# Performance work log

Measured on AMD Instinct MI355X. Metric: run time of the kernel, lower is better.

The kernel has to match this reference:

```python
import jax, jax.numpy as jnp
import numpy as np

BETA = 0.5
N = 4096

def setup_inputs() -> dict:
    key = jax.random.key(0)
    k1, k2, k3 = jax.random.split(key, 3)
    A = jax.random.uniform(k1, (N, N), dtype=jnp.float32)
    h = jax.random.normal(k2, (N, N), dtype=jnp.float32)
    W = jax.random.normal(k3, (N, N), dtype=jnp.float32) * (1.0 / np.sqrt(N))
    return {"A": A, "h": h, "W": W}

def reference(A, h, W):
    # degrees from original A (before self-loops); D = diag(deg) + I is diagonal,
    # so torch.inverse(D) == elementwise reciprocal 1/(deg+1)
    deg = jnp.sum(A, axis=1)                       # [N]
    inv_d = 1.0 / (deg + 1.0)                      # [N]
    A_I = A + jnp.eye(A.shape[0], dtype=A.dtype)   # A += I
    # A_st = (A+I) @ diag(inv_d): scale columns
    A_st = A_I * inv_d[None, :]                    # [N,N]
    # A_st_11 = A_st @ h is dead code in the original (never used) -> skipped
    temp = BETA * h + (1.0 - BETA) * A_st          # [N,N]
    return temp @ W                                # [N,N]
```

## Files before the change

### kernel.cpp

```cpp
#include <hip/hip_runtime.h>
#include <hip/hip_bf16.h>

typedef unsigned short u16;
typedef unsigned int u32;
typedef __attribute__((ext_vector_type(8))) short bf16x8;
typedef __attribute__((ext_vector_type(4))) short s16x4;
typedef __attribute__((ext_vector_type(4))) float f32x4;

#define NN 4096

__device__ __forceinline__ u16 f2bf(float f) {
    union { float f; u32 u; } v; v.f = f;
    u32 r = v.u + 0x7fffu + ((v.u >> 16) & 1u);
    return (u16)(r >> 16);
}

__global__ void rowsum_kernel(const float* __restrict__ A, float* __restrict__ invd) {
    const int row = blockIdx.x;
    const float4* a4 = reinterpret_cast<const float4*>(A + (size_t)row * NN);
    float s = 0.f;
    #pragma unroll
    for (int i = 0; i < 4; ++i) {
        float4 v = a4[threadIdx.x + i * 256];
        s += v.x + v.y + v.z + v.w;
    }
    #pragma unroll
    for (int off = 32; off > 0; off >>= 1) s += __shfl_down(s, off, 64);
    __shared__ float ws[4];
    if ((threadIdx.x & 63) == 0) ws[threadIdx.x >> 6] = s;
    __syncthreads();
    if (threadIdx.x == 0) {
        float t = ws[0] + ws[1] + ws[2] + ws[3];
        invd[row] = 1.0f / (t + 1.0f);
    }
}

__global__ void make_temp_kernel(const float* __restrict__ A, const float* __restrict__ h,
                                 const float* __restrict__ invd, u16* __restrict__ T) {
    const size_t g = ((size_t)blockIdx.x * 256 + threadIdx.x) * 8;
    const int row = (int)(g >> 12);
    const int col = (int)(g & 4095);
    const float4* a4 = reinterpret_cast<const float4*>(A + g);
    const float4* h4 = reinterpret_cast<const float4*>(h + g);
    const float4* d4 = reinterpret_cast<const float4*>(invd + col);
    float4 a0 = a4[0], a1 = a4[1];
    float4 h0 = h4[0], h1 = h4[1];
    float4 dd0 = d4[0], dd1 = d4[1];
    float av[8] = {a0.x,a0.y,a0.z,a0.w,a1.x,a1.y,a1.z,a1.w};
    float hv[8] = {h0.x,h0.y,h0.z,h0.w,h1.x,h1.y,h1.z,h1.w};
    float dv[8] = {dd0.x,dd0.y,dd0.z,dd0.w,dd1.x,dd1.y,dd1.z,dd1.w};
    bf16x8 o;
    #pragma unroll
    for (int j = 0; j < 8; ++j) {
        float aa = av[j] + ((col + j == row) ? 1.0f : 0.0f);
        float t = 0.5f * hv[j] + 0.5f * aa * dv[j];
        o[j] = (short)f2bf(t);
    }
    *reinterpret_cast<bf16x8*>(T + g) = o;
}

__global__ void transposeW_kernel(const float* __restrict__ W, u16* __restrict__ Wt) {
    __shared__ float tile[64][65];
    const int nt = blockIdx.x & 63;
    const int kt = blockIdx.x >> 6;
    const int k0 = kt * 64, n0 = nt * 64;
    const int tr = threadIdx.x >> 4;
    const int tc = (threadIdx.x & 15) * 4;
    #pragma unroll
    for (int rr = 0; rr < 64; rr += 16) {
        float4 v = *reinterpret_cast<const float4*>(&W[(size_t)(k0 + tr + rr) * NN + n0 + tc]);
        tile[tr + rr][tc + 0] = v.x;
        tile[tr + rr][tc + 1] = v.y;
        tile[tr + rr][tc + 2] = v.z;
        tile[tr + rr][tc + 3] = v.w;
    }
    __syncthreads();
    #pragma unroll
    for (int rr = 0; rr < 64; rr += 16) {
        const int n = tr + rr;
        s16x4 o;
        #pragma unroll
        for (int j = 0; j < 4; ++j) o[j] = (short)f2bf(tile[tc + j][n]);
        *reinterpret_cast<s16x4*>(&Wt[(size_t)(n0 + n) * NN + k0 + tc]) = o;
    }
}


#define GLD16(g, l) __builtin_amdgcn_global_load_lds( \
    (const __attribute__((address_space(1))) void*)(g), \
    (__attribute__((address_space(3))) void*)(l), 16, 0, 0)

__global__ __launch_bounds__(512, 2) void gemm_kernel(
    const u16* __restrict__ Atl,
    const u16* __restrict__ Btl,
    float* __restrict__ C)
{
    __shared__ u16 S[4][2][8192];

    const int tid  = threadIdx.x;
    const int wid  = tid >> 6;
    const int lane = tid & 63;
    const int llo  = lane & 15;
    const int lhi  = lane >> 4;
    const int wr   = wid >> 2;
    const int wc   = wid & 3;

    const int swz = ((int)blockIdx.x & 7) * 32 + ((int)blockIdx.x >> 3);
    const int bm = swz >> 4, bn = swz & 15;
    const int tileRow = bm * 256, tileCol = bn * 256;

    const int r0 = tid >> 2;
    const int kc = (((tid & 3) ^ ((r0 >> 1) & 3)) << 3);
    const u16* gA0 = Atl + (size_t)(tileRow + r0) * NN + kc;
    const u16* gA1 = gA0 + (size_t)128 * NN;
    const u16* gB0 = Btl + (size_t)(tileCol + r0) * NN + kc;
    const u16* gB1 = gB0 + (size_t)128 * NN;

    int offA[8], offB[4];
    #pragma unroll
    for (int m = 0; m < 8; ++m) {
        const int row = wr * 128 + m * 16 + llo;
        offA[m] = row * 32 + ((lhi ^ ((row >> 1) & 3)) << 3);
    }
    #pragma unroll
    for (int n = 0; n < 4; ++n) {
        const int row = wc * 64 + n * 16 + llo;
        offB[n] = row * 32 + ((lhi ^ ((row >> 1) & 3)) << 3);
    }

    f32x4 acc[8][4];
    #pragma unroll
    for (int m = 0; m < 8; ++m)
        #pragma unroll
        for (int n = 0; n < 4; ++n)
            acc[m][n] = (f32x4){0.f, 0.f, 0.f, 0.f};

    #pragma unroll
    for (int p = 0; p < 3; ++p) {
        GLD16(gA0 + p * 32, &S[p][0][wid * 512]);
        GLD16(gA1 + p * 32, &S[p][0][4096 + wid * 512]);
        GLD16(gB0 + p * 32, &S[p][1][wid * 512]);
        GLD16(gB1 + p * 32, &S[p][1][4096 + wid * 512]);
    }
    gA0 += 96; gA1 += 96; gB0 += 96; gB1 += 96;
    asm volatile("s_waitcnt vmcnt(8)" ::: "memory");
    __builtin_amdgcn_s_barrier();
    asm volatile("" ::: "memory");

    #pragma unroll 1
    for (int t = 0; t < 128; ++t) {
        if (t < 125) {
            const int b3 = (t + 3) & 3;
            GLD16(gA0, &S[b3][0][wid * 512]);
            GLD16(gA1, &S[b3][0][4096 + wid * 512]);
            GLD16(gB0, &S[b3][1][wid * 512]);
            GLD16(gB1, &S[b3][1][4096 + wid * 512]);
            gA0 += 32; gA1 += 32; gB0 += 32; gB1 += 32;
        }
        __builtin_amdgcn_sched_barrier(0);

        const int b = t & 3;
        const u16* sA = &S[b][0][0];
        const u16* sB = &S[b][1][0];
        bf16x8 af[8], bv[4];
        #pragma unroll
        for (int m = 0; m < 8; ++m)
            af[m] = *reinterpret_cast<const bf16x8*>(sA + offA[m]);
        #pragma unroll
        for (int n = 0; n < 4; ++n)
            bv[n] = *reinterpret_cast<const bf16x8*>(sB + offB[n]);

        __builtin_amdgcn_s_setprio(1);
        #pragma unroll
        for (int m = 0; m < 8; ++m)
            #pragma unroll
            for (int n = 0; n < 4; ++n)
                acc[m][n] = __builtin_amdgcn_mfma_f32_16x16x32_bf16(
                    af[m], bv[n], acc[m][n], 0, 0, 0);
        __builtin_amdgcn_s_setprio(0);

        if (t < 125)       asm volatile("s_waitcnt vmcnt(8)" ::: "memory");
        else if (t == 125) asm volatile("s_waitcnt vmcnt(4)" ::: "memory");
        else if (t == 126) asm volatile("s_waitcnt vmcnt(0)" ::: "memory");
        if (t < 127) {
            __builtin_amdgcn_s_barrier();
            asm volatile("" ::: "memory");
        }
    }

    #pragma unroll
    for (int m = 0; m < 8; ++m) {
        #pragma unroll
        for (int n = 0; n < 4; ++n) {
            const size_t rbase = (size_t)(tileRow + wr * 128 + m * 16 + lhi * 4) * NN
                               + tileCol + wc * 64 + n * 16 + llo;
            #pragma unroll
            for (int j = 0; j < 4; ++j)
                C[rbase + (size_t)j * NN] = acc[m][n][j];
        }
    }
}

extern "C" void kernel_launch(void* const* d_in, const int* in_sizes, int n_in,
                              void* d_out, int out_size, void* d_ws, size_t ws_size,
                              hipStream_t stream) {
    const float* A = (const float*)d_in[0];
    const float* h = (const float*)d_in[1];
    const float* W = (const float*)d_in[2];
    float* out = (float*)d_out;

    float* invd = (float*)d_ws;
    u16* temp = (u16*)((char*)d_ws + 16384);
    u16* wt   = temp + (size_t)NN * NN;

    rowsum_kernel<<<NN, 256, 0, stream>>>(A, invd);
    make_temp_kernel<<<(NN * (size_t)NN) / (256 * 8), 256, 0, stream>>>(A, h, invd, temp);
    transposeW_kernel<<<(NN / 64) * (NN / 64), 256, 0, stream>>>(W, wt);
    gemm_kernel<<<256, 512, 0, stream>>>(temp, wt, out);
}
```

Measured before the change: 176.8 us.

## Restructure GEMM main loop into four-phase ping-pong with BK=64 staging

```diff
diff --git a/kernel.cpp b/kernel.cpp
--- a/kernel.cpp
+++ b/kernel.cpp
@@ -90,12 +90,23 @@
     (const __attribute__((address_space(1))) void*)(g), \
     (__attribute__((address_space(3))) void*)(l), 16, 0, 0)
 
+#define PHASE_MID  do { __builtin_amdgcn_sched_barrier(0); \
+    __builtin_amdgcn_s_barrier(); asm volatile("" ::: "memory"); } while (0)
+#define PHASE_END  do { __builtin_amdgcn_s_barrier(); \
+    asm volatile("" ::: "memory"); } while (0)
+
+__device__ __forceinline__ bf16x8 rd(const u16* base, int off, int ks) {
+    const u16* p = base + off;
+    if (ks) p = (const u16*)((uintptr_t)p ^ 64u);
+    return *reinterpret_cast<const bf16x8*>(p);
+}
+
 __global__ __launch_bounds__(512, 2) void gemm_kernel(
     const u16* __restrict__ Atl,
     const u16* __restrict__ Btl,
     float* __restrict__ C)
 {
-    __shared__ u16 S[4][2][8192];
+    __shared__ u16 S[2][4][8192];
 
     const int tid  = threadIdx.x;
     const int wid  = tid >> 6;
@@ -109,23 +120,28 @@
     const int bm = swz >> 4, bn = swz & 15;
     const int tileRow = bm * 256, tileCol = bn * 256;
 
-    const int r0 = tid >> 2;
-    const int kc = (((tid & 3) ^ ((r0 >> 1) & 3)) << 3);
-    const u16* gA0 = Atl + (size_t)(tileRow + r0) * NN + kc;
-    const u16* gA1 = gA0 + (size_t)128 * NN;
-    const u16* gB0 = Btl + (size_t)(tileCol + r0) * NN + kc;
-    const u16* gB1 = gB0 + (size_t)128 * NN;
+    const int srow = tid >> 3;
+    const int skg  = (((tid & 7) ^ ((tid >> 4) & 7)) << 3);
+    const size_t R64  = (size_t)64 * NN;
+    const size_t R128 = (size_t)128 * NN;
+    const u16* pA = Atl + (size_t)(tileRow + srow) * NN + skg;
+    const u16* pB = Btl + (size_t)(tileCol + srow) * NN + skg;
+    u16* Sb = (u16*)&S[0][0][0];
+
+    #define STAGE(src, dstbase) do { \
+        GLD16((src), (dstbase) + tid * 8); \
+        GLD16((src) + R64, (dstbase) + 4096 + tid * 8); } while (0)
 
     int offA[8], offB[4];
     #pragma unroll
     for (int m = 0; m < 8; ++m) {
-        const int row = wr * 128 + m * 16 + llo;
-        offA[m] = row * 32 + ((lhi ^ ((row >> 1) & 3)) << 3);
+        const int row = m * 16 + llo;
+        offA[m] = row * 64 + ((lhi ^ ((row >> 1) & 7)) << 3);
     }
     #pragma unroll
     for (int n = 0; n < 4; ++n) {
-        const int row = wc * 64 + n * 16 + llo;
-        offB[n] = row * 32 + ((lhi ^ ((row >> 1) & 3)) << 3);
+        const int row = (wc & 1) * 64 + n * 16 + llo;
+        offB[n] = row * 64 + ((lhi ^ ((row >> 1) & 7)) << 3);
     }
 
     f32x4 acc[8][4];
@@ -135,57 +151,90 @@
         for (int n = 0; n < 4; ++n)
             acc[m][n] = (f32x4){0.f, 0.f, 0.f, 0.f};
 
-    #pragma unroll
-    for (int p = 0; p < 3; ++p) {
-        GLD16(gA0 + p * 32, &S[p][0][wid * 512]);
-        GLD16(gA1 + p * 32, &S[p][0][4096 + wid * 512]);
-        GLD16(gB0 + p * 32, &S[p][1][wid * 512]);
-        GLD16(gB1 + p * 32, &S[p][1][4096 + wid * 512]);
-    }
-    gA0 += 96; gA1 += 96; gB0 += 96; gB1 += 96;
-    asm volatile("s_waitcnt vmcnt(8)" ::: "memory");
+    STAGE(pA,               Sb + 0 * 8192);
+    STAGE(pA + R128,        Sb + 1 * 8192);
+    STAGE(pB,               Sb + 2 * 8192);
+    STAGE(pB + R128,        Sb + 3 * 8192);
+    STAGE(pB + 64,          Sb + 32768 + 2 * 8192);
+    STAGE(pB + R128 + 64,   Sb + 32768 + 3 * 8192);
+    asm volatile("s_waitcnt vmcnt(4)" ::: "memory");
     __builtin_amdgcn_s_barrier();
     asm volatile("" ::: "memory");
 
+    const u16* pAs = pA + 64;
+    const u16* pBs = pB + 128;
+
     #pragma unroll 1
-    for (int t = 0; t < 128; ++t) {
-        if (t < 125) {
-            const int b3 = (t + 3) & 3;
-            GLD16(gA0, &S[b3][0][wid * 512]);
-            GLD16(gA1, &S[b3][0][4096 + wid * 512]);
-            GLD16(gB0, &S[b3][1][wid * 512]);
-            GLD16(gB1, &S[b3][1][4096 + wid * 512]);
-            gA0 += 32; gA1 += 32; gB0 += 32; gB1 += 32;
-        }
-        __builtin_amdgcn_sched_barrier(0);
-
-        const int b = t & 3;
-        const u16* sA = &S[b][0][0];
-        const u16* sB = &S[b][1][0];
-        bf16x8 af[8], bv[4];
-        #pragma unroll
-        for (int m = 0; m < 8; ++m)
-            af[m] = *reinterpret_cast<const bf16x8*>(sA + offA[m]);
-        #pragma unroll
-        for (int n = 0; n < 4; ++n)
-            bv[n] = *reinterpret_cast<const bf16x8*>(sB + offB[n]);
-
-        __builtin_amdgcn_s_setprio(1);
-        #pragma unroll
-        for (int m = 0; m < 8; ++m)
-            #pragma unroll
-            for (int n = 0; n < 4; ++n)
-                acc[m][n] = __builtin_amdgcn_mfma_f32_16x16x32_bf16(
-                    af[m], bv[n], acc[m][n], 0, 0, 0);
-        __builtin_amdgcn_s_setprio(0);
-
-        if (t < 125)       asm volatile("s_waitcnt vmcnt(8)" ::: "memory");
-        else if (t == 125) asm volatile("s_waitcnt vmcnt(4)" ::: "memory");
-        else if (t == 126) asm volatile("s_waitcnt vmcnt(0)" ::: "memory");
-        if (t < 127) {
-            __builtin_amdgcn_s_barrier();
-            asm volatile("" ::: "memory");
-        }
+    for (int g = 0; g < 64; ++g) {
+        u16* cb = Sb + (g & 1) * 32768;
+        u16* nbuf = Sb + ((g + 1) & 1) * 32768;
+        const u16* sAr = cb + wr * 8192;
+        const u16* sBr = cb + (2 + (wc >> 1)) * 8192;
+
+        bf16x8 a0[4][2], a1[4][2], b0[2][2], b1[2][2];
+        #pragma unroll
+        for (int m = 0; m < 4; ++m) { a0[m][0] = rd(sAr, offA[m], 0); a0[m][1] = rd(sAr, offA[m], 1); }
+        #pragma unroll
+        for (int n = 0; n < 2; ++n) { b0[n][0] = rd(sBr, offB[n], 0); b0[n][1] = rd(sBr, offB[n], 1); }
+        if (g < 63) STAGE(pAs, nbuf + 0 * 8192);
+        PHASE_MID;
+        __builtin_amdgcn_s_setprio(1);
+        #pragma unroll
+        for (int ks = 0; ks < 2; ++ks)
+            #pragma unroll
+            for (int m = 0; m < 4; ++m)
+                #pragma unroll
+                for (int n = 0; n < 2; ++n)
+                    acc[m][n] = __builtin_amdgcn_mfma_f32_16x16x32_bf16(a0[m][ks], b0[n][ks], acc[m][n], 0, 0, 0);
+        __builtin_amdgcn_s_setprio(0);
+        PHASE_END;
+
+        #pragma unroll
+        for (int n = 0; n < 2; ++n) { b1[n][0] = rd(sBr, offB[2 + n], 0); b1[n][1] = rd(sBr, offB[2 + n], 1); }
+        if (g < 63) STAGE(pAs + R128, nbuf + 1 * 8192);
+        PHASE_MID;
+        __builtin_amdgcn_s_setprio(1);
+        #pragma unroll
+        for (int ks = 0; ks < 2; ++ks)
+            #pragma unroll
+            for (int m = 0; m < 4; ++m)
+                #pragma unroll
+                for (int n = 0; n < 2; ++n)
+                    acc[m][2 + n] = __builtin_amdgcn_mfma_f32_16x16x32_bf16(a0[m][ks], b1[n][ks], acc[m][2 + n], 0, 0, 0);
+        __builtin_amdgcn_s_setprio(0);
+        PHASE_END;
+
+        #pragma unroll
+        for (int m = 0; m < 4; ++m) { a1[m][0] = rd(sAr, offA[4 + m], 0); a1[m][1] = rd(sAr, offA[4 + m], 1); }
+        if (g < 62) STAGE(pBs, cb + 2 * 8192);
+        PHASE_MID;
+        __builtin_amdgcn_s_setprio(1);
+        #pragma unroll
+        for (int ks = 0; ks < 2; ++ks)
+            #pragma unroll
+            for (int m = 0; m < 4; ++m)
+                #pragma unroll
+                for (int n = 0; n < 2; ++n)
+                    acc[4 + m][n] = __builtin_amdgcn_mfma_f32_16x16x32_bf16(a1[m][ks], b0[n][ks], acc[4 + m][n], 0, 0, 0);
+        __builtin_amdgcn_s_setprio(0);
+        PHASE_END;
+
+        if (g < 62) STAGE(pBs + R128, cb + 3 * 8192);
+        if (g < 62)       asm volatile("s_waitcnt vmcnt(4)" ::: "memory");
+        else if (g == 62) asm volatile("s_waitcnt vmcnt(0)" ::: "memory");
+        PHASE_MID;
+        __builtin_amdgcn_s_setprio(1);
+        #pragma unroll
+        for (int ks = 0; ks < 2; ++ks)
+            #pragma unroll
+            for (int m = 0; m < 4; ++m)
+                #pragma unroll
+                for (int n = 0; n < 2; ++n)
+                    acc[4 + m][2 + n] = __builtin_amdgcn_mfma_f32_16x16x32_bf16(a1[m][ks], b1[n][ks], acc[4 + m][2 + n], 0, 0, 0);
+        __builtin_amdgcn_s_setprio(0);
+        if (g < 63) PHASE_END;
+
+        pAs += 64; pBs += 64;
     }
 
     #pragma unroll
@@ -199,6 +248,7 @@
                 C[rbase + (size_t)j * NN] = acc[m][n][j];
         }
     }
+    #undef STAGE
 }
 
 extern "C" void kernel_launch(void* const* d_in, const int* in_sizes, int n_in,
```

Measured after the change: 235.3 us. 33.1% more time.

## Switch GEMM to double-buffered BK=64 tiles with two MFMA k-steps

Applied to the files above, without the earlier changes.

```diff
diff --git a/kernel.cpp b/kernel.cpp
--- a/kernel.cpp
+++ b/kernel.cpp
@@ -95,7 +95,7 @@
     const u16* __restrict__ Btl,
     float* __restrict__ C)
 {
-    __shared__ u16 S[4][2][8192];
+    __shared__ u16 S[2][2][16384];
 
     const int tid  = threadIdx.x;
     const int wid  = tid >> 6;
@@ -109,23 +109,23 @@
     const int bm = swz >> 4, bn = swz & 15;
     const int tileRow = bm * 256, tileCol = bn * 256;
 
-    const int r0 = tid >> 2;
-    const int kc = (((tid & 3) ^ ((r0 >> 1) & 3)) << 3);
-    const u16* gA0 = Atl + (size_t)(tileRow + r0) * NN + kc;
-    const u16* gA1 = gA0 + (size_t)128 * NN;
-    const u16* gB0 = Btl + (size_t)(tileCol + r0) * NN + kc;
-    const u16* gB1 = gB0 + (size_t)128 * NN;
+    const int r0 = tid >> 3;
+    const int kc = (((tid & 7) ^ (r0 & 7)) << 3);
+    const size_t R128 = (size_t)128 * NN;
+    const u16* gA = Atl + (size_t)(tileRow + r0) * NN + kc;
+    const u16* gB = Btl + (size_t)(tileCol + r0) * NN + kc;
+
 
     int offA[8], offB[4];
     #pragma unroll
     for (int m = 0; m < 8; ++m) {
         const int row = wr * 128 + m * 16 + llo;
-        offA[m] = row * 32 + ((lhi ^ ((row >> 1) & 3)) << 3);
+        offA[m] = row * 64 + ((lhi ^ (row & 7)) << 3);
     }
     #pragma unroll
     for (int n = 0; n < 4; ++n) {
         const int row = wc * 64 + n * 16 + llo;
-        offB[n] = row * 32 + ((lhi ^ ((row >> 1) & 3)) << 3);
+        offB[n] = row * 64 + ((lhi ^ (row & 7)) << 3);
     }
 
     f32x4 acc[8][4];
@@ -135,40 +135,35 @@
         for (int n = 0; n < 4; ++n)
             acc[m][n] = (f32x4){0.f, 0.f, 0.f, 0.f};
 
-    #pragma unroll
-    for (int p = 0; p < 3; ++p) {
-        GLD16(gA0 + p * 32, &S[p][0][wid * 512]);
-        GLD16(gA1 + p * 32, &S[p][0][4096 + wid * 512]);
-        GLD16(gB0 + p * 32, &S[p][1][wid * 512]);
-        GLD16(gB1 + p * 32, &S[p][1][4096 + wid * 512]);
-    }
-    gA0 += 96; gA1 += 96; gB0 += 96; gB1 += 96;
-    asm volatile("s_waitcnt vmcnt(8)" ::: "memory");
+    #define STAGE_TILE(buf, koff) do { \
+        _Pragma("unroll") \
+        for (int i = 0; i < 4; ++i) { \
+            GLD16(gA + (size_t)(i * 64) * NN + (koff), &S[buf][0][i * 4096 + tid * 8]); \
+            GLD16(gB + (size_t)(i * 64) * NN + (koff), &S[buf][1][i * 4096 + tid * 8]); \
+        } } while (0)
+
+    STAGE_TILE(0, 0);
+    asm volatile("s_waitcnt vmcnt(0)" ::: "memory");
     __builtin_amdgcn_s_barrier();
     asm volatile("" ::: "memory");
 
     #pragma unroll 1
-    for (int t = 0; t < 128; ++t) {
-        if (t < 125) {
-            const int b3 = (t + 3) & 3;
-            GLD16(gA0, &S[b3][0][wid * 512]);
-            GLD16(gA1, &S[b3][0][4096 + wid * 512]);
-            GLD16(gB0, &S[b3][1][wid * 512]);
-            GLD16(gB1, &S[b3][1][4096 + wid * 512]);
-            gA0 += 32; gA1 += 32; gB0 += 32; gB1 += 32;
+    for (int t = 0; t < 64; ++t) {
+        if (t < 63) STAGE_TILE((t + 1) & 1, (t + 1) * 64);
+        __builtin_amdgcn_sched_barrier(0);
+
+        const u16* sA = &S[t & 1][0][0];
+        const u16* sB = &S[t & 1][1][0];
+
+        bf16x8 bv[4][2], af[8];
+        #pragma unroll
+        for (int n = 0; n < 4; ++n) {
+            bv[n][0] = *reinterpret_cast<const bf16x8*>(sB + offB[n]);
+            bv[n][1] = *reinterpret_cast<const bf16x8*>(sB + (offB[n] ^ 32));
         }
-        __builtin_amdgcn_sched_barrier(0);
-
-        const int b = t & 3;
-        const u16* sA = &S[b][0][0];
-        const u16* sB = &S[b][1][0];
-        bf16x8 af[8], bv[4];
         #pragma unroll
         for (int m = 0; m < 8; ++m)
             af[m] = *reinterpret_cast<const bf16x8*>(sA + offA[m]);
-        #pragma unroll
-        for (int n = 0; n < 4; ++n)
-            bv[n] = *reinterpret_cast<const bf16x8*>(sB + offB[n]);
 
         __builtin_amdgcn_s_setprio(1);
         #pragma unroll
@@ -176,17 +171,29 @@
             #pragma unroll
             for (int n = 0; n < 4; ++n)
                 acc[m][n] = __builtin_amdgcn_mfma_f32_16x16x32_bf16(
-                    af[m], bv[n], acc[m][n], 0, 0, 0);
+                    af[m], bv[n][0], acc[m][n], 0, 0, 0);
         __builtin_amdgcn_s_setprio(0);
 
-        if (t < 125)       asm volatile("s_waitcnt vmcnt(8)" ::: "memory");
-        else if (t == 125) asm volatile("s_waitcnt vmcnt(4)" ::: "memory");
-        else if (t == 126) asm volatile("s_waitcnt vmcnt(0)" ::: "memory");
-        if (t < 127) {
+        #pragma unroll
+        for (int m = 0; m < 8; ++m)
+            af[m] = *reinterpret_cast<const bf16x8*>(sA + (offA[m] ^ 32));
+
+        __builtin_amdgcn_s_setprio(1);
+        #pragma unroll
+        for (int m = 0; m < 8; ++m)
+            #pragma unroll
+            for (int n = 0; n < 4; ++n)
+                acc[m][n] = __builtin_amdgcn_mfma_f32_16x16x32_bf16(
+                    af[m], bv[n][1], acc[m][n], 0, 0, 0);
+        __builtin_amdgcn_s_setprio(0);
+
+        if (t < 63) {
+            asm volatile("s_waitcnt vmcnt(0)" ::: "memory");
             __builtin_amdgcn_s_barrier();
             asm volatile("" ::: "memory");
         }
     }
+    #undef STAGE_TILE
 
     #pragma unroll
     for (int m = 0; m < 8; ++m) {
```

Result: faster. 168.2 us (-4.9%).

## Double-buffer GEMM fragments in registers with a three-stage LDS ring

Applied to the files above, without the earlier changes.

```diff
diff --git a/kernel.cpp b/kernel.cpp
--- a/kernel.cpp
+++ b/kernel.cpp
@@ -95,7 +95,8 @@
     const u16* __restrict__ Btl,
     float* __restrict__ C)
 {
-    __shared__ u16 S[4][2][8192];
+    __shared__ u16 SA[3][8192];
+    __shared__ u16 SB[3][8192];
 
     const int tid  = threadIdx.x;
     const int wid  = tid >> 6;
@@ -111,10 +112,15 @@
 
     const int r0 = tid >> 2;
     const int kc = (((tid & 3) ^ ((r0 >> 1) & 3)) << 3);
-    const u16* gA0 = Atl + (size_t)(tileRow + r0) * NN + kc;
-    const u16* gA1 = gA0 + (size_t)128 * NN;
-    const u16* gB0 = Btl + (size_t)(tileCol + r0) * NN + kc;
-    const u16* gB1 = gB0 + (size_t)128 * NN;
+    const size_t R128 = (size_t)128 * NN;
+    const u16* gA = Atl + (size_t)(tileRow + r0) * NN + kc;
+    const u16* gB = Btl + (size_t)(tileCol + r0) * NN + kc;
+
+    #define STAGE(WB, KOFF) do { \
+        GLD16(gA + (KOFF),        &SA[WB][tid * 8]); \
+        GLD16(gA + R128 + (KOFF), &SA[WB][4096 + tid * 8]); \
+        GLD16(gB + (KOFF),        &SB[WB][tid * 8]); \
+        GLD16(gB + R128 + (KOFF), &SB[WB][4096 + tid * 8]); } while (0)
 
     int offA[8], offB[4];
     #pragma unroll
@@ -135,58 +141,69 @@
         for (int n = 0; n < 4; ++n)
             acc[m][n] = (f32x4){0.f, 0.f, 0.f, 0.f};
 
-    #pragma unroll
-    for (int p = 0; p < 3; ++p) {
-        GLD16(gA0 + p * 32, &S[p][0][wid * 512]);
-        GLD16(gA1 + p * 32, &S[p][0][4096 + wid * 512]);
-        GLD16(gB0 + p * 32, &S[p][1][wid * 512]);
-        GLD16(gB1 + p * 32, &S[p][1][4096 + wid * 512]);
-    }
-    gA0 += 96; gA1 += 96; gB0 += 96; gB1 += 96;
-    asm volatile("s_waitcnt vmcnt(8)" ::: "memory");
+    bf16x8 aE[8], bE[4], aO[8], bO[4];
+
+    STAGE(0, 0);
+    STAGE(1, 32);
+    asm volatile("s_waitcnt vmcnt(4)" ::: "memory");
     __builtin_amdgcn_s_barrier();
     asm volatile("" ::: "memory");
+    #pragma unroll
+    for (int m = 0; m < 8; ++m) aE[m] = *reinterpret_cast<const bf16x8*>(&SA[0][0] + offA[m]);
+    #pragma unroll
+    for (int n = 0; n < 4; ++n) bE[n] = *reinterpret_cast<const bf16x8*>(&SB[0][0] + offB[n]);
+
+    int wb = 2;
+    int rb = 1;
+    int koff = 64;
+
+    #define STEP(SG, VM0, RD, AC, BC, AN, BN) do { \
+        if (SG) { STAGE(wb, koff); koff += 32; } \
+        if (VM0) asm volatile("s_waitcnt vmcnt(0)" ::: "memory"); \
+        else     asm volatile("s_waitcnt vmcnt(4)" ::: "memory"); \
+        __builtin_amdgcn_s_barrier(); \
+        asm volatile("" ::: "memory"); \
+        const u16* rA = &SA[rb][0]; \
+        const u16* rB = &SB[rb][0]; \
+        if (RD) { \
+            _Pragma("unroll") \
+            for (int m = 0; m < 4; ++m) AN[m] = *reinterpret_cast<const bf16x8*>(rA + offA[m]); \
+        } \
+        __builtin_amdgcn_sched_barrier(0); \
+        __builtin_amdgcn_s_setprio(1); \
+        _Pragma("unroll") \
+        for (int m = 0; m < 4; ++m) \
+            _Pragma("unroll") \
+            for (int n = 0; n < 4; ++n) \
+                acc[m][n] = __builtin_amdgcn_mfma_f32_16x16x32_bf16(AC[m], BC[n], acc[m][n], 0, 0, 0); \
+        __builtin_amdgcn_s_setprio(0); \
+        __builtin_amdgcn_sched_barrier(0); \
+        if (RD) { \
+            _Pragma("unroll") \
+            for (int m = 4; m < 8; ++m) AN[m] = *reinterpret_cast<const bf16x8*>(rA + offA[m]); \
+            _Pragma("unroll") \
+            for (int n = 0; n < 4; ++n) BN[n] = *reinterpret_cast<const bf16x8*>(rB + offB[n]); \
+        } \
+        __builtin_amdgcn_sched_barrier(0); \
+        __builtin_amdgcn_s_setprio(1); \
+        _Pragma("unroll") \
+        for (int m = 4; m < 8; ++m) \
+            _Pragma("unroll") \
+            for (int n = 0; n < 4; ++n) \
+                acc[m][n] = __builtin_amdgcn_mfma_f32_16x16x32_bf16(AC[m], BC[n], acc[m][n], 0, 0, 0); \
+        __builtin_amdgcn_s_setprio(0); \
+        rb = (rb == 2) ? 0 : rb + 1; \
+        wb = (wb == 2) ? 0 : wb + 1; \
+    } while (0)
 
     #pragma unroll 1
-    for (int t = 0; t < 128; ++t) {
-        if (t < 125) {
-            const int b3 = (t + 3) & 3;
-            GLD16(gA0, &S[b3][0][wid * 512]);
-            GLD16(gA1, &S[b3][0][4096 + wid * 512]);
-            GLD16(gB0, &S[b3][1][wid * 512]);
-            GLD16(gB1, &S[b3][1][4096 + wid * 512]);
-            gA0 += 32; gA1 += 32; gB0 += 32; gB1 += 32;
-        }
-        __builtin_amdgcn_sched_barrier(0);
-
-        const int b = t & 3;
-        const u16* sA = &S[b][0][0];
-        const u16* sB = &S[b][1][0];
-        bf16x8 af[8], bv[4];
-        #pragma unroll
-        for (int m = 0; m < 8; ++m)
-            af[m] = *reinterpret_cast<const bf16x8*>(sA + offA[m]);
-        #pragma unroll
-        for (int n = 0; n < 4; ++n)
-            bv[n] = *reinterpret_cast<const bf16x8*>(sB + offB[n]);
-
-        __builtin_amdgcn_s_setprio(1);
-        #pragma unroll
-        for (int m = 0; m < 8; ++m)
-            #pragma unroll
-            for (int n = 0; n < 4; ++n)
-                acc[m][n] = __builtin_amdgcn_mfma_f32_16x16x32_bf16(
-                    af[m], bv[n], acc[m][n], 0, 0, 0);
-        __builtin_amdgcn_s_setprio(0);
-
-        if (t < 125)       asm volatile("s_waitcnt vmcnt(8)" ::: "memory");
-        else if (t == 125) asm volatile("s_waitcnt vmcnt(4)" ::: "memory");
-        else if (t == 126) asm volatile("s_waitcnt vmcnt(0)" ::: "memory");
-        if (t < 127) {
-            __builtin_amdgcn_s_barrier();
-            asm volatile("" ::: "memory");
-        }
-    }
+    for (int tt = 0; tt < 64; ++tt) {
+        const bool sg = tt < 63;
+        STEP(sg, !sg, true, aE, bE, aO, bO);
+        STEP(sg, !sg && false, sg, aO, bO, aE, bE);
+    }
+    #undef STEP
+    #undef STAGE
 
     #pragma unroll
     for (int m = 0; m < 8; ++m) {
```

New measurement: 179.0 us. Within noise of the previous version (+1.2%).
